# Performance work log

Measured on AMD Instinct MI355X. Metric: run time of the kernel, lower is better.

## Reference

```python
import jax, jax.numpy as jnp
import numpy as np

N = 20000
E = 640000
IN_DIM = 128
HID = 128
OUT = 64


def setup_inputs() -> dict:
    key = jax.random.key(0)
    ks = jax.random.split(key, 16)
    s = 0.05
    inp = {
        'feat': jax.random.normal(ks[0], (N, IN_DIM), jnp.float32),
        'edge_index': jax.random.randint(ks[1], (2, E), 0, N, jnp.int64),
        # GCNConv params
        'W_gcn': jax.random.normal(ks[2], (IN_DIM, HID), jnp.float32) * s,
        'b_gcn': jnp.zeros((HID,), jnp.float32),
        # SAGEConv params (lin_l: aggregated neighbors w/ bias; lin_r: root, no bias)
        'W_sage_l': jax.random.normal(ks[3], (HID, HID), jnp.float32) * s,
        'b_sage_l': jnp.zeros((HID,), jnp.float32),
        'W_sage_r': jax.random.normal(ks[4], (HID, HID), jnp.float32) * s,
        # policy MLP
        'W1': jax.random.normal(ks[5], (HID, HID), jnp.float32) * s,
        'b1': jnp.zeros((HID,), jnp.float32),
        'W2': jax.random.normal(ks[6], (HID, HID), jnp.float32) * s,
        'b2': jnp.zeros((HID,), jnp.float32),
        'W3': jax.random.normal(ks[7], (HID, OUT), jnp.float32) * s,
        'b3': jnp.zeros((OUT,), jnp.float32),
        # value head
        'Wv': jax.random.normal(ks[8], (HID, 1), jnp.float32) * s,
        'bv': jnp.zeros((1,), jnp.float32),
    }
    return inp


def _gcn(feat, src, dst, W, b):
    # PyG GCNConv: add self loops, sym-normalize by deg^-1/2 on both ends
    loop = jnp.arange(N, dtype=src.dtype)
    s = jnp.concatenate([src, loop])
    d = jnp.concatenate([dst, loop])
    deg = jax.ops.segment_sum(jnp.ones_like(d, jnp.float32), d, num_segments=N)
    dinv = jnp.where(deg > 0, jax.lax.rsqrt(deg), 0.0)
    x = feat @ W  # [N, HID]
    msg = x[s] * (dinv[s] * dinv[d])[:, None]  # [E+N, HID]
    return jax.ops.segment_sum(msg, d, num_segments=N) + b


def _sage_mean(h, src, dst, Wl, bl, Wr):
    # PyG SAGEConv(aggr='mean'): lin_l(mean_neigh) + lin_r(root)
    neigh_sum = jax.ops.segment_sum(h[src], dst, num_segments=N)
    cnt = jax.ops.segment_sum(jnp.ones_like(dst, jnp.float32), dst, num_segments=N)
    mean = neigh_sum / jnp.maximum(cnt, 1.0)[:, None]
    return mean @ Wl + bl + h @ Wr


def reference(feat, edge_index, W_gcn, b_gcn, W_sage_l, b_sage_l, W_sage_r,
              W1, b1, W2, b2, W3, b3, Wv, bv):
    src, dst = edge_index[0], edge_index[1]
    h = jax.nn.relu(_gcn(feat, src, dst, W_gcn, b_gcn))
    h = jax.nn.relu(_sage_mean(h, src, dst, W_sage_l, b_sage_l, W_sage_r))
    # policy MLP (GELU exact, matching torch nn.GELU default)
    z = jax.nn.gelu(h @ W1 + b1, approximate=False)
    z = jax.nn.gelu(z @ W2 + b2, approximate=False)
    means = z @ W3 + b3  # [N, OUT]
    values = (h @ Wv + bv)[:, 0]  # [N]
    return (means, values)
```

## Files before the change

### kernel.cpp

```cpp
#include <hip/hip_runtime.h>
#include <math.h>


typedef __attribute__((ext_vector_type(8))) short short8;
typedef __attribute__((ext_vector_type(4))) float floatx4;

__device__ __forceinline__ unsigned short f2b(float f) {
    unsigned u = __float_as_uint(f);
    unsigned r = (u + 0x7fffu + ((u >> 16) & 1u)) >> 16;
    return (unsigned short)r;
}
__device__ __forceinline__ float b2f(unsigned short h) {
    return __uint_as_float(((unsigned)h) << 16);
}
__device__ __forceinline__ float b2f_lo(unsigned v) {
    return __uint_as_float(v << 16);
}
__device__ __forceinline__ float b2f_hi(unsigned v) {
    return __uint_as_float(v & 0xffff0000u);
}
__device__ __forceinline__ floatx4 MFMA(short8 a, short8 b, floatx4 c) {
    return __builtin_amdgcn_mfma_f32_16x16x32_bf16(a, b, c, 0, 0, 0);
}
__device__ __forceinline__ float gelu_exact(float x) {
    return 0.5f * x * (1.0f + erff(x * 0.70710678118654752440f));
}

#define FRAG(P, ct, ks, lane) (*(const short8*)((P) + (((((ct)*4 + (ks))*64) + (lane)) << 3)))


__global__ __launch_bounds__(256) void count_pack_kernel(
    const int* __restrict__ eidx, int E,
    int* __restrict__ cnt, int* __restrict__ rank,
    const float* Wg, const float* Wsl, const float* Wsr,
    const float* W1, const float* W2, const float* W3,
    unsigned short* Pg, unsigned short* Psl, unsigned short* Psr,
    unsigned short* P1, unsigned short* P2, unsigned short* P3,
    int countBlocks)
{
    if ((int)blockIdx.x < countBlocks) {
        int e = blockIdx.x * 256 + threadIdx.x;
        if (e < E) {
            int d = eidx[E + e];
            rank[e] = atomicAdd(&cnt[d], 1);
        }
        return;
    }
    int t = (blockIdx.x - countBlocks) * 256 + threadIdx.x;
    const float* W; unsigned short* P; int NC = 128; int base;
    if (t < 2048)       { W = Wg;  P = Pg;  base = t; }
    else if (t < 4096)  { W = Wsl; P = Psl; base = t - 2048; }
    else if (t < 6144)  { W = Wsr; P = Psr; base = t - 4096; }
    else if (t < 8192)  { W = W1;  P = P1;  base = t - 6144; }
    else if (t < 10240) { W = W2;  P = P2;  base = t - 8192; }
    else if (t < 11264) { W = W3;  P = P3;  base = t - 10240; NC = 64; }
    else return;
    int l  = base & 63;
    int ks = (base >> 6) & 3;
    int ct = base >> 8;
    int n  = ct * 16 + (l & 15);
    int k0 = ks * 32 + ((l >> 4) << 3);
    short8 v;
    #pragma unroll
    for (int j = 0; j < 8; j++) v[j] = (short)f2b(W[(size_t)(k0 + j) * NC + n]);
    *(short8*)(P + ((size_t)base << 3)) = v;
}


__global__ __launch_bounds__(256) void scanA_gemm_kernel(
    const int* __restrict__ cnt, int N,
    int* __restrict__ row_ptr, int* __restrict__ blocksums, int scanBlocks,
    const float* __restrict__ feat, const unsigned short* __restrict__ Pg,
    unsigned short* __restrict__ xs, int M)
{
    if ((int)blockIdx.x < scanBlocks) {
        __shared__ int sh[256];
        int b = blockIdx.x, tid = threadIdx.x;
        int i0 = b * 1024 + tid * 4;
        int v0 = (i0 + 0 < N) ? cnt[i0 + 0] : 0;
        int v1 = (i0 + 1 < N) ? cnt[i0 + 1] : 0;
        int v2 = (i0 + 2 < N) ? cnt[i0 + 2] : 0;
        int v3 = (i0 + 3 < N) ? cnt[i0 + 3] : 0;
        int tot = v0 + v1 + v2 + v3;
        sh[tid] = tot;
        __syncthreads();
        for (int off = 1; off < 256; off <<= 1) {
            int t = (tid >= off) ? sh[tid - off] : 0;
            __syncthreads();
            sh[tid] += t;
            __syncthreads();
        }
        int excl = sh[tid] - tot;
        if (i0 + 0 < N) row_ptr[i0 + 0] = excl;
        if (i0 + 1 < N) row_ptr[i0 + 1] = excl + v0;
        if (i0 + 2 < N) row_ptr[i0 + 2] = excl + v0 + v1;
        if (i0 + 3 < N) row_ptr[i0 + 3] = excl + v0 + v1 + v2;
        if (tid == 255) blocksums[b] = sh[255];
        return;
    }
    int bid = blockIdx.x - scanBlocks;
    int w = bid * 4 + (threadIdx.x >> 6);
    if (w >= (M / 16) * 2) return;
    int lane = threadIdx.x & 63;
    int m = lane & 15, quad = lane >> 4;
    int rt = w >> 1, ch = w & 1;
    const float* arow = feat + (size_t)(rt * 16 + m) * 128;
    short8 a[4];
    #pragma unroll
    for (int ks = 0; ks < 4; ks++) {
        float4 f0 = *(const float4*)(arow + ks * 32 + quad * 8);
        float4 f1 = *(const float4*)(arow + ks * 32 + quad * 8 + 4);
        short8 s;
        s[0] = (short)f2b(f0.x); s[1] = (short)f2b(f0.y);
        s[2] = (short)f2b(f0.z); s[3] = (short)f2b(f0.w);
        s[4] = (short)f2b(f1.x); s[5] = (short)f2b(f1.y);
        s[6] = (short)f2b(f1.z); s[7] = (short)f2b(f1.w);
        a[ks] = s;
    }
    #pragma unroll
    for (int ct = 0; ct < 4; ct++) {
        floatx4 acc = {0.f, 0.f, 0.f, 0.f};
        #pragma unroll
        for (int ks = 0; ks < 4; ks++)
            acc = MFMA(a[ks], FRAG(Pg, ch * 4 + ct, ks, lane), acc);
        #pragma unroll
        for (int reg = 0; reg < 4; reg++)
            xs[(size_t)(rt * 16 + quad * 4 + reg) * 128 + (ch * 4 + ct) * 16 + m] =
                f2b(acc[reg]);
    }
}


__global__ __launch_bounds__(256) void scanC_kernel(
    const int* __restrict__ cnt, const int* __restrict__ blocksums,
    int N, int E, int* __restrict__ row_ptr,
    float* __restrict__ dinv, float* __restrict__ rcnt)
{
    int b = blockIdx.x, tid = threadIdx.x;
    int offset = 0;
    for (int j = 0; j < b; j++) offset += blocksums[j];
    int i0 = b * 1024 + tid * 4;
    #pragma unroll
    for (int q = 0; q < 4; q++) {
        int i = i0 + q;
        if (i < N) {
            row_ptr[i] += offset;
            int c = cnt[i];
            dinv[i] = rsqrtf((float)(c + 1));
            rcnt[i] = 1.0f / (float)(c > 0 ? c : 1);
        }
    }
    if (b == 0 && tid == 0) row_ptr[N] = E;
}


__global__ void fill_kernel(const int* __restrict__ eidx, const int* __restrict__ rank,
                            const int* __restrict__ row_ptr, int E, int* __restrict__ col)
{
    int e = blockIdx.x * blockDim.x + threadIdx.x;
    if (e < E) {
        int d = eidx[E + e];
        col[row_ptr[d] + rank[e]] = eidx[e];
    }
}


template<bool GCN>
__global__ __launch_bounds__(256) void agg_kernel(
    const unsigned short* __restrict__ X, const int* __restrict__ row_ptr,
    const int* __restrict__ col, const float* __restrict__ dinv,
    const float* __restrict__ rcnt, const float* __restrict__ bias,
    unsigned short* __restrict__ Y, int N)
{
    int w = (int)((blockIdx.x * 256 + threadIdx.x) >> 6);
    int lane = threadIdx.x & 63;
    if (w >= N) return;
    const unsigned* Xu = (const unsigned*)X;
    float ax = 0.f, ay = 0.f;
    if (GCN) {
        unsigned v = Xu[(size_t)w * 64 + lane];
        float dv = dinv[w];
        ax = b2f_lo(v) * dv;
        ay = b2f_hi(v) * dv;
    }
    int beg = row_ptr[w], end = row_ptr[w + 1];
    for (int base = beg; base < end; base += 64) {
        int rem = end - base;
        int n = rem < 64 ? rem : 64;
        int idx = (lane < n) ? col[base + lane] : 0;
        int j = 0;
        for (; j + 4 <= n; j += 4) {
            int s0 = __shfl(idx, j);
            int s1 = __shfl(idx, j + 1);
            int s2 = __shfl(idx, j + 2);
            int s3 = __shfl(idx, j + 3);
            unsigned v0 = Xu[(size_t)s0 * 64 + lane];
            unsigned v1 = Xu[(size_t)s1 * 64 + lane];
            unsigned v2 = Xu[(size_t)s2 * 64 + lane];
            unsigned v3 = Xu[(size_t)s3 * 64 + lane];
            if (GCN) {
                float d0 = dinv[s0], d1 = dinv[s1], d2 = dinv[s2], d3 = dinv[s3];
                ax = fmaf(b2f_lo(v0), d0, ax); ay = fmaf(b2f_hi(v0), d0, ay);
                ax = fmaf(b2f_lo(v1), d1, ax); ay = fmaf(b2f_hi(v1), d1, ay);
                ax = fmaf(b2f_lo(v2), d2, ax); ay = fmaf(b2f_hi(v2), d2, ay);
                ax = fmaf(b2f_lo(v3), d3, ax); ay = fmaf(b2f_hi(v3), d3, ay);
            } else {
                ax += b2f_lo(v0) + b2f_lo(v1) + b2f_lo(v2) + b2f_lo(v3);
                ay += b2f_hi(v0) + b2f_hi(v1) + b2f_hi(v2) + b2f_hi(v3);
            }
        }
        for (; j < n; j++) {
            int s = __shfl(idx, j);
            unsigned v = Xu[(size_t)s * 64 + lane];
            if (GCN) {
                float d = dinv[s];
                ax = fmaf(b2f_lo(v), d, ax); ay = fmaf(b2f_hi(v), d, ay);
            } else {
                ax += b2f_lo(v); ay += b2f_hi(v);
            }
        }
    }
    float ox, oy;
    if (GCN) {
        float dv = dinv[w];
        float2 b = ((const float2*)bias)[lane];
        ox = fmaxf(fmaf(ax, dv, b.x), 0.f);
        oy = fmaxf(fmaf(ay, dv, b.y), 0.f);
    } else {
        float rc = rcnt[w];
        ox = ax * rc;
        oy = ay * rc;
    }
    unsigned out = (unsigned)f2b(ox) | ((unsigned)f2b(oy) << 16);
    ((unsigned*)Y)[(size_t)w * 64 + lane] = out;
}


__global__ __launch_bounds__(256) void sage_gemm_kernel(
    const unsigned short* __restrict__ mean, const unsigned short* __restrict__ h1,
    const unsigned short* __restrict__ Psl, const unsigned short* __restrict__ Psr,
    const float* __restrict__ bsl, unsigned short* __restrict__ h2, int M)
{
    int w = blockIdx.x * 4 + (threadIdx.x >> 6);
    if (w >= (M / 16) * 2) return;
    int lane = threadIdx.x & 63;
    int m = lane & 15, quad = lane >> 4;
    int rt = w >> 1, ch = w & 1;
    short8 am[4], ar[4];
    #pragma unroll
    for (int ks = 0; ks < 4; ks++) {
        am[ks] = *(const short8*)(mean + (size_t)(rt * 16 + m) * 128 + ks * 32 + quad * 8);
        ar[ks] = *(const short8*)(h1   + (size_t)(rt * 16 + m) * 128 + ks * 32 + quad * 8);
    }
    #pragma unroll
    for (int ct = 0; ct < 4; ct++) {
        floatx4 acc = {0.f, 0.f, 0.f, 0.f};
        int gct = ch * 4 + ct;
        #pragma unroll
        for (int ks = 0; ks < 4; ks++) acc = MFMA(am[ks], FRAG(Psl, gct, ks, lane), acc);
        #pragma unroll
        for (int ks = 0; ks < 4; ks++) acc = MFMA(ar[ks], FRAG(Psr, gct, ks, lane), acc);
        float bb = bsl[gct * 16 + m];
        #pragma unroll
        for (int reg = 0; reg < 4; reg++)
            h2[(size_t)(rt * 16 + quad * 4 + reg) * 128 + gct * 16 + m] =
                f2b(fmaxf(acc[reg] + bb, 0.f));
    }
}


__global__ __launch_bounds__(256) void mlp_kernel(
    const unsigned short* __restrict__ h2,
    const unsigned short* __restrict__ P1, const float* __restrict__ b1,
    const unsigned short* __restrict__ P2, const float* __restrict__ b2,
    const unsigned short* __restrict__ P3, const float* __restrict__ b3,
    const float* __restrict__ Wv, const float* __restrict__ bv,
    float* __restrict__ means, float* __restrict__ values, int M)
{
    __shared__ unsigned short z[4][16 * 136];
    int widx = threadIdx.x >> 6, lane = threadIdx.x & 63;
    int w = blockIdx.x * 4 + widx;
    if (w >= M / 16) return;
    int m = lane & 15, quad = lane >> 4;
    unsigned short* zt = &z[widx][0];
    int r0 = w * 16;

    short8 a[4];
    #pragma unroll
    for (int ks = 0; ks < 4; ks++)
        a[ks] = *(const short8*)(h2 + (size_t)(r0 + m) * 128 + ks * 32 + quad * 8);

    float p = 0.f;
    #pragma unroll
    for (int ks = 0; ks < 4; ks++) {
        const float* wvp = Wv + ks * 32 + quad * 8;
        float4 w0 = *(const float4*)wvp;
        float4 w1 = *(const float4*)(wvp + 4);
        p = fmaf(b2f((unsigned short)a[ks][0]), w0.x, p);
        p = fmaf(b2f((unsigned short)a[ks][1]), w0.y, p);
        p = fmaf(b2f((unsigned short)a[ks][2]), w0.z, p);
        p = fmaf(b2f((unsigned short)a[ks][3]), w0.w, p);
        p = fmaf(b2f((unsigned short)a[ks][4]), w1.x, p);
        p = fmaf(b2f((unsigned short)a[ks][5]), w1.y, p);
        p = fmaf(b2f((unsigned short)a[ks][6]), w1.z, p);
        p = fmaf(b2f((unsigned short)a[ks][7]), w1.w, p);
    }
    p += __shfl_xor(p, 16);
    p += __shfl_xor(p, 32);
    if (lane < 16) values[r0 + m] = p + bv[0];

    #pragma unroll
    for (int ct = 0; ct < 8; ct++) {
        floatx4 acc = {0.f, 0.f, 0.f, 0.f};
        #pragma unroll
        for (int ks = 0; ks < 4; ks++) acc = MFMA(a[ks], FRAG(P1, ct, ks, lane), acc);
        float bb = b1[ct * 16 + m];
        #pragma unroll
        for (int reg = 0; reg < 4; reg++)
            zt[(quad * 4 + reg) * 136 + ct * 16 + m] = f2b(gelu_exact(acc[reg] + bb));
    }
    short8 a2[4];
    #pragma unroll
    for (int ks = 0; ks < 4; ks++)
        a2[ks] = *(const short8*)(zt + m * 136 + ks * 32 + quad * 8);

    #pragma unroll
    for (int ct = 0; ct < 8; ct++) {
        floatx4 acc = {0.f, 0.f, 0.f, 0.f};
        #pragma unroll
        for (int ks = 0; ks < 4; ks++) acc = MFMA(a2[ks], FRAG(P2, ct, ks, lane), acc);
        float bb = b2[ct * 16 + m];
        #pragma unroll
        for (int reg = 0; reg < 4; reg++)
            zt[(quad * 4 + reg) * 136 + ct * 16 + m] = f2b(gelu_exact(acc[reg] + bb));
    }
    short8 a3[4];
    #pragma unroll
    for (int ks = 0; ks < 4; ks++)
        a3[ks] = *(const short8*)(zt + m * 136 + ks * 32 + quad * 8);

    #pragma unroll
    for (int ct = 0; ct < 4; ct++) {
        floatx4 acc = {0.f, 0.f, 0.f, 0.f};
        #pragma unroll
        for (int ks = 0; ks < 4; ks++) acc = MFMA(a3[ks], FRAG(P3, ct, ks, lane), acc);
        float bb = b3[ct * 16 + m];
        #pragma unroll
        for (int reg = 0; reg < 4; reg++)
            means[(size_t)(r0 + quad * 4 + reg) * 64 + ct * 16 + m] = acc[reg] + bb;
    }
}


extern "C" void kernel_launch(void* const* d_in, const int* in_sizes, int n_in,
                              void* d_out, int out_size, void* d_ws, size_t ws_size,
                              hipStream_t stream) {
    const float* feat  = (const float*)d_in[0];
    const int*   eidx  = (const int*)d_in[1];
    const float* W_gcn = (const float*)d_in[2];
    const float* b_gcn = (const float*)d_in[3];
    const float* W_sl  = (const float*)d_in[4];
    const float* b_sl  = (const float*)d_in[5];
    const float* W_sr  = (const float*)d_in[6];
    const float* W1    = (const float*)d_in[7];
    const float* b1    = (const float*)d_in[8];
    const float* W2    = (const float*)d_in[9];
    const float* b2    = (const float*)d_in[10];
    const float* W3    = (const float*)d_in[11];
    const float* b3    = (const float*)d_in[12];
    const float* Wv    = (const float*)d_in[13];
    const float* bv    = (const float*)d_in[14];

    const int N = in_sizes[0] / 128;
    const int E = in_sizes[1] / 2;

    char* ws = (char*)d_ws;
    size_t off = 0;
    auto alloc = [&](size_t bytes) -> void* {
        void* p = ws + off;
        off += (bytes + 255) & ~(size_t)255;
        return p;
    };
    int*   cnt     = (int*)alloc((size_t)N * 4);
    int*   rank    = (int*)alloc((size_t)E * 4);
    int*   row_ptr = (int*)alloc((size_t)(N + 1) * 4);
    int*   bsums   = (int*)alloc(32 * 4);
    float* dinv    = (float*)alloc((size_t)N * 4);
    float* rcnt    = (float*)alloc((size_t)N * 4);
    int*   col     = (int*)alloc((size_t)E * 4);
    unsigned short* xs   = (unsigned short*)alloc((size_t)N * 128 * 2);
    unsigned short* h1   = (unsigned short*)alloc((size_t)N * 128 * 2);
    unsigned short* mean = (unsigned short*)alloc((size_t)N * 128 * 2);
    unsigned short* h2   = (unsigned short*)alloc((size_t)N * 128 * 2);
    unsigned short* Pg   = (unsigned short*)alloc(2048 * 8 * 2);
    unsigned short* Psl  = (unsigned short*)alloc(2048 * 8 * 2);
    unsigned short* Psr  = (unsigned short*)alloc(2048 * 8 * 2);
    unsigned short* P1   = (unsigned short*)alloc(2048 * 8 * 2);
    unsigned short* P2   = (unsigned short*)alloc(2048 * 8 * 2);
    unsigned short* P3   = (unsigned short*)alloc(1024 * 8 * 2);

    hipMemsetAsync(cnt, 0, (size_t)N * 4, stream);

    const int countBlocks = (E + 255) / 256;
    const int packBlocks  = (11264 + 255) / 256;
    count_pack_kernel<<<countBlocks + packBlocks, 256, 0, stream>>>(
        eidx, E, cnt, rank, W_gcn, W_sl, W_sr, W1, W2, W3,
        Pg, Psl, Psr, P1, P2, P3, countBlocks);

    const int NB = (N + 1023) / 1024;
    const int gcnBlocks = ((N / 16) * 2 + 3) / 4;
    scanA_gemm_kernel<<<NB + gcnBlocks, 256, 0, stream>>>(
        cnt, N, row_ptr, bsums, NB, feat, Pg, xs, N);

    scanC_kernel<<<NB, 256, 0, stream>>>(cnt, bsums, N, E, row_ptr, dinv, rcnt);

    fill_kernel<<<(E + 255) / 256, 256, 0, stream>>>(eidx, rank, row_ptr, E, col);

    const int agrid = (N + 3) / 4;
    agg_kernel<true><<<agrid, 256, 0, stream>>>(xs, row_ptr, col, dinv, rcnt, b_gcn, h1, N);
    agg_kernel<false><<<agrid, 256, 0, stream>>>(h1, row_ptr, col, dinv, rcnt, nullptr, mean, N);

    sage_gemm_kernel<<<gcnBlocks, 256, 0, stream>>>(mean, h1, Psl, Psr, b_sl, h2, N);

    mlp_kernel<<<(N / 16 + 3) / 4, 256, 0, stream>>>(
        h2, P1, b1, P2, b2, P3, b3, Wv, bv,
        (float*)d_out, (float*)d_out + (size_t)N * 64, N);
}
```

Measured before the change: 205.1 us.

## Fuse scan fixup into consumers, fuse SAGE GEMM into MLP, vectorize aggregation

Drops the separate scan-fixup kernel: fill and aggregation now add the per-block offsets from bsums on the fly, and dinv is computed during the scan. The fill pass is merged with the GCN GEMM launch, and the SAGE GEMM is fused into the MLP kernel, which removes the h2 round trip through global memory. The aggregation kernel now has each wave gather four neighbors at once with 16-byte loads per lane and reduces across lane groups with shuffles. The cost is that every thread rescans the bsums prefix, and the values head is now reduced inside the fused kernel.

Result: faster. 200.5 us (-2.3%).

```diff
diff --git a/kernel.cpp b/kernel.cpp
--- a/kernel.cpp
+++ b/kernel.cpp
@@ -67,38 +67,55 @@
 }
 
 
-__global__ __launch_bounds__(256) void scanA_gemm_kernel(
+__global__ __launch_bounds__(256) void scan_kernel(
     const int* __restrict__ cnt, int N,
-    int* __restrict__ row_ptr, int* __restrict__ blocksums, int scanBlocks,
+    int* __restrict__ row_ptr, int* __restrict__ bsums,
+    float* __restrict__ dinv)
+{
+    __shared__ int sh[256];
+    int b = blockIdx.x, tid = threadIdx.x;
+    int i0 = b * 1024 + tid * 4;
+    int v0 = (i0 + 0 < N) ? cnt[i0 + 0] : 0;
+    int v1 = (i0 + 1 < N) ? cnt[i0 + 1] : 0;
+    int v2 = (i0 + 2 < N) ? cnt[i0 + 2] : 0;
+    int v3 = (i0 + 3 < N) ? cnt[i0 + 3] : 0;
+    int tot = v0 + v1 + v2 + v3;
+    sh[tid] = tot;
+    __syncthreads();
+    for (int off = 1; off < 256; off <<= 1) {
+        int t = (tid >= off) ? sh[tid - off] : 0;
+        __syncthreads();
+        sh[tid] += t;
+        __syncthreads();
+    }
+    int excl = sh[tid] - tot;
+    if (i0 + 0 < N) { row_ptr[i0 + 0] = excl;                dinv[i0 + 0] = rsqrtf((float)(v0 + 1)); }
+    if (i0 + 1 < N) { row_ptr[i0 + 1] = excl + v0;           dinv[i0 + 1] = rsqrtf((float)(v1 + 1)); }
+    if (i0 + 2 < N) { row_ptr[i0 + 2] = excl + v0 + v1;      dinv[i0 + 2] = rsqrtf((float)(v2 + 1)); }
+    if (i0 + 3 < N) { row_ptr[i0 + 3] = excl + v0 + v1 + v2; dinv[i0 + 3] = rsqrtf((float)(v3 + 1)); }
+    if (tid == 255) bsums[b] = sh[255];
+}
+
+
+__global__ __launch_bounds__(256) void fill_gemm_kernel(
+    const int* __restrict__ eidx, const int* __restrict__ rank,
+    const int* __restrict__ row_ptr, const int* __restrict__ bsums,
+    int E, int* __restrict__ col,
     const float* __restrict__ feat, const unsigned short* __restrict__ Pg,
-    unsigned short* __restrict__ xs, int M)
+    unsigned short* __restrict__ xs, int M, int fillBlocks)
 {
-    if ((int)blockIdx.x < scanBlocks) {
-        __shared__ int sh[256];
-        int b = blockIdx.x, tid = threadIdx.x;
-        int i0 = b * 1024 + tid * 4;
-        int v0 = (i0 + 0 < N) ? cnt[i0 + 0] : 0;
-        int v1 = (i0 + 1 < N) ? cnt[i0 + 1] : 0;
-        int v2 = (i0 + 2 < N) ? cnt[i0 + 2] : 0;
-        int v3 = (i0 + 3 < N) ? cnt[i0 + 3] : 0;
-        int tot = v0 + v1 + v2 + v3;
-        sh[tid] = tot;
-        __syncthreads();
-        for (int off = 1; off < 256; off <<= 1) {
-            int t = (tid >= off) ? sh[tid - off] : 0;
-            __syncthreads();
-            sh[tid] += t;
-            __syncthreads();
+    if ((int)blockIdx.x < fillBlocks) {
+        int e = blockIdx.x * 256 + threadIdx.x;
+        if (e < E) {
+            int d = eidx[E + e];
+            int b = d >> 10;
+            int off = 0;
+            for (int j = 0; j < b; j++) off += bsums[j];
+            col[off + row_ptr[d] + rank[e]] = eidx[e];
         }
-        int excl = sh[tid] - tot;
-        if (i0 + 0 < N) row_ptr[i0 + 0] = excl;
-        if (i0 + 1 < N) row_ptr[i0 + 1] = excl + v0;
-        if (i0 + 2 < N) row_ptr[i0 + 2] = excl + v0 + v1;
-        if (i0 + 3 < N) row_ptr[i0 + 3] = excl + v0 + v1 + v2;
-        if (tid == 255) blocksums[b] = sh[255];
         return;
     }
-    int bid = blockIdx.x - scanBlocks;
+    int bid = blockIdx.x - fillBlocks;
     int w = bid * 4 + (threadIdx.x >> 6);
     if (w >= (M / 16) * 2) return;
     int lane = threadIdx.x & 63;
@@ -131,146 +148,103 @@
 }
 
 
-__global__ __launch_bounds__(256) void scanC_kernel(
-    const int* __restrict__ cnt, const int* __restrict__ blocksums,
-    int N, int E, int* __restrict__ row_ptr,
-    float* __restrict__ dinv, float* __restrict__ rcnt)
-{
-    int b = blockIdx.x, tid = threadIdx.x;
-    int offset = 0;
-    for (int j = 0; j < b; j++) offset += blocksums[j];
-    int i0 = b * 1024 + tid * 4;
-    #pragma unroll
-    for (int q = 0; q < 4; q++) {
-        int i = i0 + q;
-        if (i < N) {
-            row_ptr[i] += offset;
-            int c = cnt[i];
-            dinv[i] = rsqrtf((float)(c + 1));
-            rcnt[i] = 1.0f / (float)(c > 0 ? c : 1);
-        }
-    }
-    if (b == 0 && tid == 0) row_ptr[N] = E;
-}
-
-
-__global__ void fill_kernel(const int* __restrict__ eidx, const int* __restrict__ rank,
-                            const int* __restrict__ row_ptr, int E, int* __restrict__ col)
-{
-    int e = blockIdx.x * blockDim.x + threadIdx.x;
-    if (e < E) {
-        int d = eidx[E + e];
-        col[row_ptr[d] + rank[e]] = eidx[e];
-    }
-}
-
-
 template<bool GCN>
 __global__ __launch_bounds__(256) void agg_kernel(
     const unsigned short* __restrict__ X, const int* __restrict__ row_ptr,
-    const int* __restrict__ col, const float* __restrict__ dinv,
-    const float* __restrict__ rcnt, const float* __restrict__ bias,
-    unsigned short* __restrict__ Y, int N)
+    const int* __restrict__ bsums, const int* __restrict__ col,
+    const float* __restrict__ dinv, const float* __restrict__ bias,
+    unsigned short* __restrict__ Y, int N, int E)
 {
     int w = (int)((blockIdx.x * 256 + threadIdx.x) >> 6);
+    if (w >= N) return;
     int lane = threadIdx.x & 63;
-    if (w >= N) return;
-    const unsigned* Xu = (const unsigned*)X;
-    float ax = 0.f, ay = 0.f;
-    if (GCN) {
-        unsigned v = Xu[(size_t)w * 64 + lane];
-        float dv = dinv[w];
-        ax = b2f_lo(v) * dv;
-        ay = b2f_hi(v) * dv;
-    }
-    int beg = row_ptr[w], end = row_ptr[w + 1];
+    int g = lane >> 4, t = lane & 15;
+    const uint4* Xq = (const uint4*)X;
+
+    int b = w >> 10;
+    int off = 0;
+    for (int j = 0; j < b; j++) off += bsums[j];
+    int beg = off + row_ptr[w];
+    int end;
+    if (w + 1 < N) {
+        int off2 = (((w + 1) >> 10) != b) ? off + bsums[b] : off;
+        end = off2 + row_ptr[w + 1];
+    } else end = E;
+    int deg = end - beg;
+
+    float acc[8] = {0.f, 0.f, 0.f, 0.f, 0.f, 0.f, 0.f, 0.f};
+
     for (int base = beg; base < end; base += 64) {
         int rem = end - base;
         int n = rem < 64 ? rem : 64;
         int idx = (lane < n) ? col[base + lane] : 0;
-        int j = 0;
-        for (; j + 4 <= n; j += 4) {
-            int s0 = __shfl(idx, j);
-            int s1 = __shfl(idx, j + 1);
-            int s2 = __shfl(idx, j + 2);
-            int s3 = __shfl(idx, j + 3);
-            unsigned v0 = Xu[(size_t)s0 * 64 + lane];
-            unsigned v1 = Xu[(size_t)s1 * 64 + lane];
-            unsigned v2 = Xu[(size_t)s2 * 64 + lane];
-            unsigned v3 = Xu[(size_t)s3 * 64 + lane];
-            if (GCN) {
-                float d0 = dinv[s0], d1 = dinv[s1], d2 = dinv[s2], d3 = dinv[s3];
-                ax = fmaf(b2f_lo(v0), d0, ax); ay = fmaf(b2f_hi(v0), d0, ay);
-                ax = fmaf(b2f_lo(v1), d1, ax); ay = fmaf(b2f_hi(v1), d1, ay);
-                ax = fmaf(b2f_lo(v2), d2, ax); ay = fmaf(b2f_hi(v2), d2, ay);
-                ax = fmaf(b2f_lo(v3), d3, ax); ay = fmaf(b2f_hi(v3), d3, ay);
-            } else {
-                ax += b2f_lo(v0) + b2f_lo(v1) + b2f_lo(v2) + b2f_lo(v3);
-                ay += b2f_hi(v0) + b2f_hi(v1) + b2f_hi(v2) + b2f_hi(v3);
+        for (int j0 = 0; j0 < n; j0 += 16) {
+            #pragma unroll
+            for (int u = 0; u < 4; u++) {
+                int j = j0 + u * 4 + g;
+                int s = __shfl(idx, j & 63);
+                if (j < n) {
+                    uint4 q = Xq[(size_t)s * 16 + t];
+                    float sc = GCN ? dinv[s] : 1.0f;
+                    acc[0] = fmaf(b2f_lo(q.x), sc, acc[0]);
+                    acc[1] = fmaf(b2f_hi(q.x), sc, acc[1]);
+                    acc[2] = fmaf(b2f_lo(q.y), sc, acc[2]);
+                    acc[3] = fmaf(b2f_hi(q.y), sc, acc[3]);
+                    acc[4] = fmaf(b2f_lo(q.z), sc, acc[4]);
+                    acc[5] = fmaf(b2f_hi(q.z), sc, acc[5]);
+                    acc[6] = fmaf(b2f_lo(q.w), sc, acc[6]);
+                    acc[7] = fmaf(b2f_hi(q.w), sc, acc[7]);
+                }
             }
         }
-        for (; j < n; j++) {
-            int s = __shfl(idx, j);
-            unsigned v = Xu[(size_t)s * 64 + lane];
-            if (GCN) {
-                float d = dinv[s];
-                ax = fmaf(b2f_lo(v), d, ax); ay = fmaf(b2f_hi(v), d, ay);
-            } else {
-                ax += b2f_lo(v); ay += b2f_hi(v);
-            }
+    }
+    #pragma unroll
+    for (int i = 0; i < 8; i++) {
+        acc[i] += __shfl_xor(acc[i], 16);
+        acc[i] += __shfl_xor(acc[i], 32);
+    }
+    if (g == 0) {
+        float out[8];
+        if (GCN) {
+            float dw = dinv[w];
+            uint4 q = Xq[(size_t)w * 16 + t];
+            acc[0] = fmaf(b2f_lo(q.x), dw, acc[0]);
+            acc[1] = fmaf(b2f_hi(q.x), dw, acc[1]);
+            acc[2] = fmaf(b2f_lo(q.y), dw, acc[2]);
+            acc[3] = fmaf(b2f_hi(q.y), dw, acc[3]);
+            acc[4] = fmaf(b2f_lo(q.z), dw, acc[4]);
+            acc[5] = fmaf(b2f_hi(q.z), dw, acc[5]);
+            acc[6] = fmaf(b2f_lo(q.w), dw, acc[6]);
+            acc[7] = fmaf(b2f_hi(q.w), dw, acc[7]);
+            float4 b0 = *(const float4*)(bias + t * 8);
+            float4 b1 = *(const float4*)(bias + t * 8 + 4);
+            out[0] = fmaxf(fmaf(acc[0], dw, b0.x), 0.f);
+            out[1] = fmaxf(fmaf(acc[1], dw, b0.y), 0.f);
+            out[2] = fmaxf(fmaf(acc[2], dw, b0.z), 0.f);
+            out[3] = fmaxf(fmaf(acc[3], dw, b0.w), 0.f);
+            out[4] = fmaxf(fmaf(acc[4], dw, b1.x), 0.f);
+            out[5] = fmaxf(fmaf(acc[5], dw, b1.y), 0.f);
+            out[6] = fmaxf(fmaf(acc[6], dw, b1.z), 0.f);
+            out[7] = fmaxf(fmaf(acc[7], dw, b1.w), 0.f);
+        } else {
+            float rc = 1.0f / (float)(deg > 0 ? deg : 1);
+            #pragma unroll
+            for (int i = 0; i < 8; i++) out[i] = acc[i] * rc;
         }
-    }
-    float ox, oy;
-    if (GCN) {
-        float dv = dinv[w];
-        float2 b = ((const float2*)bias)[lane];
-        ox = fmaxf(fmaf(ax, dv, b.x), 0.f);
-        oy = fmaxf(fmaf(ay, dv, b.y), 0.f);
-    } else {
-        float rc = rcnt[w];
-        ox = ax * rc;
-        oy = ay * rc;
-    }
-    unsigned out = (unsigned)f2b(ox) | ((unsigned)f2b(oy) << 16);
-    ((unsigned*)Y)[(size_t)w * 64 + lane] = out;
-}
-
-
-__global__ __launch_bounds__(256) void sage_gemm_kernel(
+        uint4 r;
+        r.x = (unsigned)f2b(out[0]) | ((unsigned)f2b(out[1]) << 16);
+        r.y = (unsigned)f2b(out[2]) | ((unsigned)f2b(out[3]) << 16);
+        r.z = (unsigned)f2b(out[4]) | ((unsigned)f2b(out[5]) << 16);
+        r.w = (unsigned)f2b(out[6]) | ((unsigned)f2b(out[7]) << 16);
+        ((uint4*)Y)[(size_t)w * 16 + t] = r;
+    }
+}
+
+
+__global__ __launch_bounds__(256) void sage_mlp_kernel(
     const unsigned short* __restrict__ mean, const unsigned short* __restrict__ h1,
     const unsigned short* __restrict__ Psl, const unsigned short* __restrict__ Psr,
-    const float* __restrict__ bsl, unsigned short* __restrict__ h2, int M)
-{
-    int w = blockIdx.x * 4 + (threadIdx.x >> 6);
-    if (w >= (M / 16) * 2) return;
-    int lane = threadIdx.x & 63;
-    int m = lane & 15, quad = lane >> 4;
-    int rt = w >> 1, ch = w & 1;
-    short8 am[4], ar[4];
-    #pragma unroll
-    for (int ks = 0; ks < 4; ks++) {
-        am[ks] = *(const short8*)(mean + (size_t)(rt * 16 + m) * 128 + ks * 32 + quad * 8);
-        ar[ks] = *(const short8*)(h1   + (size_t)(rt * 16 + m) * 128 + ks * 32 + quad * 8);
-    }
-    #pragma unroll
-    for (int ct = 0; ct < 4; ct++) {
-        floatx4 acc = {0.f, 0.f, 0.f, 0.f};
-        int gct = ch * 4 + ct;
-        #pragma unroll
-        for (int ks = 0; ks < 4; ks++) acc = MFMA(am[ks], FRAG(Psl, gct, ks, lane), acc);
-        #pragma unroll
-        for (int ks = 0; ks < 4; ks++) acc = MFMA(ar[ks], FRAG(Psr, gct, ks, lane), acc);
-        float bb = bsl[gct * 16 + m];
-        #pragma unroll
-        for (int reg = 0; reg < 4; reg++)
-            h2[(size_t)(rt * 16 + quad * 4 + reg) * 128 + gct * 16 + m] =
-                f2b(fmaxf(acc[reg] + bb, 0.f));
-    }
-}
-
-
-__global__ __launch_bounds__(256) void mlp_kernel(
-    const unsigned short* __restrict__ h2,
+    const float* __restrict__ bsl,
     const unsigned short* __restrict__ P1, const float* __restrict__ b1,
     const unsigned short* __restrict__ P2, const float* __restrict__ b2,
     const unsigned short* __restrict__ P3, const float* __restrict__ b3,
@@ -285,35 +259,53 @@
     unsigned short* zt = &z[widx][0];
     int r0 = w * 16;
 
-    short8 a[4];
-    #pragma unroll
-    for (int ks = 0; ks < 4; ks++)
-        a[ks] = *(const short8*)(h2 + (size_t)(r0 + m) * 128 + ks * 32 + quad * 8);
-
-    float p = 0.f;
+    short8 am[4], ar[4];
     #pragma unroll
     for (int ks = 0; ks < 4; ks++) {
-        const float* wvp = Wv + ks * 32 + quad * 8;
-        float4 w0 = *(const float4*)wvp;
-        float4 w1 = *(const float4*)(wvp + 4);
-        p = fmaf(b2f((unsigned short)a[ks][0]), w0.x, p);
-        p = fmaf(b2f((unsigned short)a[ks][1]), w0.y, p);
-        p = fmaf(b2f((unsigned short)a[ks][2]), w0.z, p);
-        p = fmaf(b2f((unsigned short)a[ks][3]), w0.w, p);
-        p = fmaf(b2f((unsigned short)a[ks][4]), w1.x, p);
-        p = fmaf(b2f((unsigned short)a[ks][5]), w1.y, p);
-        p = fmaf(b2f((unsigned short)a[ks][6]), w1.z, p);
-        p = fmaf(b2f((unsigned short)a[ks][7]), w1.w, p);
-    }
-    p += __shfl_xor(p, 16);
-    p += __shfl_xor(p, 32);
-    if (lane < 16) values[r0 + m] = p + bv[0];
-
+        am[ks] = *(const short8*)(mean + (size_t)(r0 + m) * 128 + ks * 32 + quad * 8);
+        ar[ks] = *(const short8*)(h1   + (size_t)(r0 + m) * 128 + ks * 32 + quad * 8);
+    }
+
+    float vpart[4] = {0.f, 0.f, 0.f, 0.f};
     #pragma unroll
     for (int ct = 0; ct < 8; ct++) {
         floatx4 acc = {0.f, 0.f, 0.f, 0.f};
         #pragma unroll
-        for (int ks = 0; ks < 4; ks++) acc = MFMA(a[ks], FRAG(P1, ct, ks, lane), acc);
+        for (int ks = 0; ks < 4; ks++) acc = MFMA(am[ks], FRAG(Psl, ct, ks, lane), acc);
+        #pragma unroll
+        for (int ks = 0; ks < 4; ks++) acc = MFMA(ar[ks], FRAG(Psr, ct, ks, lane), acc);
+        float bb = bsl[ct * 16 + m];
+        float wv = Wv[ct * 16 + m];
+        #pragma unroll
+        for (int reg = 0; reg < 4; reg++) {
+            float o = fmaxf(acc[reg] + bb, 0.f);
+            vpart[reg] = fmaf(o, wv, vpart[reg]);
+            zt[(quad * 4 + reg) * 136 + ct * 16 + m] = f2b(o);
+        }
+    }
+    #pragma unroll
+    for (int off = 1; off <= 8; off <<= 1) {
+        #pragma unroll
+        for (int reg = 0; reg < 4; reg++)
+            vpart[reg] += __shfl_xor(vpart[reg], off);
+    }
+    if (m == 0) {
+        float bvv = bv[0];
+        #pragma unroll
+        for (int reg = 0; reg < 4; reg++)
+            values[r0 + quad * 4 + reg] = vpart[reg] + bvv;
+    }
+
+    short8 a1[4];
+    #pragma unroll
+    for (int ks = 0; ks < 4; ks++)
+        a1[ks] = *(const short8*)(zt + m * 136 + ks * 32 + quad * 8);
+
+    #pragma unroll
+    for (int ct = 0; ct < 8; ct++) {
+        floatx4 acc = {0.f, 0.f, 0.f, 0.f};
+        #pragma unroll
+        for (int ks = 0; ks < 4; ks++) acc = MFMA(a1[ks], FRAG(P1, ct, ks, lane), acc);
         float bb = b1[ct * 16 + m];
         #pragma unroll
         for (int reg = 0; reg < 4; reg++)
@@ -383,15 +375,13 @@
     };
     int*   cnt     = (int*)alloc((size_t)N * 4);
     int*   rank    = (int*)alloc((size_t)E * 4);
-    int*   row_ptr = (int*)alloc((size_t)(N + 1) * 4);
+    int*   row_ptr = (int*)alloc((size_t)N * 4);
     int*   bsums   = (int*)alloc(32 * 4);
     float* dinv    = (float*)alloc((size_t)N * 4);
-    float* rcnt    = (float*)alloc((size_t)N * 4);
     int*   col     = (int*)alloc((size_t)E * 4);
     unsigned short* xs   = (unsigned short*)alloc((size_t)N * 128 * 2);
     unsigned short* h1   = (unsigned short*)alloc((size_t)N * 128 * 2);
     unsigned short* mean = (unsigned short*)alloc((size_t)N * 128 * 2);
-    unsigned short* h2   = (unsigned short*)alloc((size_t)N * 128 * 2);
     unsigned short* Pg   = (unsigned short*)alloc(2048 * 8 * 2);
     unsigned short* Psl  = (unsigned short*)alloc(2048 * 8 * 2);
     unsigned short* Psr  = (unsigned short*)alloc(2048 * 8 * 2);
@@ -408,21 +398,18 @@
         Pg, Psl, Psr, P1, P2, P3, countBlocks);
 
     const int NB = (N + 1023) / 1024;
-    const int gcnBlocks = ((N / 16) * 2 + 3) / 4;
-    scanA_gemm_kernel<<<NB + gcnBlocks, 256, 0, stream>>>(
-        cnt, N, row_ptr, bsums, NB, feat, Pg, xs, N);
-
-    scanC_kernel<<<NB, 256, 0, stream>>>(cnt, bsums, N, E, row_ptr, dinv, rcnt);
-
-    fill_kernel<<<(E + 255) / 256, 256, 0, stream>>>(eidx, rank, row_ptr, E, col);
+    scan_kernel<<<NB, 256, 0, stream>>>(cnt, N, row_ptr, bsums, dinv);
+
+    const int fillBlocks = (E + 255) / 256;
+    const int gemmBlocks = ((N / 16) * 2 + 3) / 4;
+    fill_gemm_kernel<<<fillBlocks + gemmBlocks, 256, 0, stream>>>(
+        eidx, rank, row_ptr, bsums, E, col, feat, Pg, xs, N, fillBlocks);
 
     const int agrid = (N + 3) / 4;
-    agg_kernel<true><<<agrid, 256, 0, stream>>>(xs, row_ptr, col, dinv, rcnt, b_gcn, h1, N);
-    agg_kernel<false><<<agrid, 256, 0, stream>>>(h1, row_ptr, col, dinv, rcnt, nullptr, mean, N);
-
-    sage_gemm_kernel<<<gcnBlocks, 256, 0, stream>>>(mean, h1, Psl, Psr, b_sl, h2, N);
-
-    mlp_kernel<<<(N / 16 + 3) / 4, 256, 0, stream>>>(
-        h2, P1, b1, P2, b2, P3, b3, Wv, bv,
+    agg_kernel<true><<<agrid, 256, 0, stream>>>(xs, row_ptr, bsums, col, dinv, b_gcn, h1, N, E);
+    agg_kernel<false><<<agrid, 256, 0, stream>>>(h1, row_ptr, bsums, col, dinv, nullptr, mean, N, E);
+
+    sage_mlp_kernel<<<(N / 16 + 3) / 4, 256, 0, stream>>>(
+        mean, h1, Psl, Psr, b_sl, P1, b1, P2, b2, P3, b3, Wv, bv,
         (float*)d_out, (float*)d_out + (size_t)N * 64, N);
 }
```
